# Kernel tuning notes

Measured on AMD Instinct MI355X. Metric: run time of the kernel, lower is better.

Reference implementation:

```python
import jax, jax.numpy as jnp
import numpy as np
import math

NUM_HEADS = 12


def _rope_tables(nph, npw, half_head_dim):
    # grid coords: x = column index, y = row index, flattened row-major
    rows = jnp.arange(nph, dtype=jnp.float32)
    cols = jnp.arange(npw, dtype=jnp.float32)
    gy, gx = jnp.meshgrid(rows, cols, indexing='ij')
    coords = jnp.stack([gx.ravel(), gy.ravel()], axis=1)  # [N, 2]
    cmin = coords.min(axis=0, keepdims=True)
    cmax = coords.max(axis=0, keepdims=True)
    nc = (coords - cmin) / (cmax - cmin + 1e-8)
    div = jnp.exp(jnp.arange(0, half_head_dim, 2, dtype=jnp.float32)
                  * (-(math.log(10000.0) / half_head_dim)))  # [half/2]
    px = nc[:, 0:1] * div  # [N, half/2]
    py = nc[:, 1:2] * div
    rep = lambda t: jnp.repeat(t, 2, axis=-1)  # interleave: even/odd slots get same value
    return rep(jnp.cos(px)), rep(jnp.sin(px)), rep(jnp.cos(py)), rep(jnp.sin(py))


def _apply_rope(t, cos_x, sin_x, cos_y, sin_y):
    # t: [B, H, N, Dh]; tables: [N, Dh//2] broadcast over B, H
    half = t.shape[-1] // 2
    tx, ty = t[..., :half], t[..., half:]
    rx = tx * cos_x + jnp.roll(tx, 1, axis=-1) * sin_x
    ry = ty * cos_y + jnp.roll(ty, 1, axis=-1) * sin_y
    return jnp.concatenate([rx, ry], axis=-1)


def setup_inputs() -> dict:
    key = jax.random.key(0)
    k1, k2, k3 = jax.random.split(key, 3)
    B, S, E = 32, 577, 768  # 24*24 patches + 1 CLS token
    x = jax.random.normal(k1, (B, S, E), dtype=jnp.float32)
    w_qkv = jax.random.normal(k2, (3 * E, E), dtype=jnp.float32) * 0.02
    w_proj = jax.random.normal(k3, (E, E), dtype=jnp.float32) * 0.02
    return {"x": x, "w_qkv": w_qkv, "w_proj": w_proj,
            "num_patches_h": 24, "num_patches_w": 24}


def reference(x, w_qkv, w_proj, num_patches_h, num_patches_w):
    B, S, E = x.shape
    H = NUM_HEADS
    Dh = E // H
    # QKV projection (bias=False)
    qkv = jnp.einsum('bse,fe->bsf', x, w_qkv).reshape(B, S, 3, H, Dh)
    qkv = jnp.transpose(qkv, (2, 0, 3, 1, 4))  # [3, B, H, S, Dh]
    q, k, v = qkv[0], qkv[1], qkv[2]
    # 2D RoPE on patch tokens only (CLS at position 0 unchanged)
    cx, sx, cy, sy = _rope_tables(num_patches_h, num_patches_w, Dh // 2)
    q_patch = _apply_rope(q[:, :, 1:], cx, sx, cy, sy)
    k_patch = _apply_rope(k[:, :, 1:], cx, sx, cy, sy)
    q = jnp.concatenate([q[:, :, :1], q_patch], axis=2)
    k = jnp.concatenate([k[:, :, :1], k_patch], axis=2)
    # scaled dot-product attention (standard backend, dropout=0)
    attn = jnp.einsum('bhqd,bhkd->bhqk', q, k) * (Dh ** -0.5)
    attn = jax.nn.softmax(attn, axis=-1)
    out = jnp.einsum('bhqk,bhkd->bhqd', attn, v)
    out = jnp.transpose(out, (0, 2, 1, 3)).reshape(B, S, E)
    return out @ w_proj.T
```

## Files before the change

### kernel.cpp

```cpp
#include <hip/hip_runtime.h>
#include <hip/hip_bf16.h>
#include <cstdint>


typedef __attribute__((ext_vector_type(8))) short bf16x8;
typedef __attribute__((ext_vector_type(4))) float f32x4;

#define MFMA16(a, b, c) __builtin_amdgcn_mfma_f32_16x16x32_bf16((a), (b), (c), 0, 0, 0)

#define S_LEN 577
#define NHEAD 12
#define DHEAD 64
#define EMB   768
#define F3    2304
#define NT_KV 10

__device__ __forceinline__ void gload_lds16(const __hip_bfloat16* g, __hip_bfloat16* l) {
    __builtin_amdgcn_global_load_lds(
        (const __attribute__((address_space(1))) unsigned int*)g,
        (__attribute__((address_space(3))) unsigned int*)l, 16, 0, 0);
}

__device__ __forceinline__ uint4 load8_f32(const float* p) {
    const float4 f0 = *(const float4*)p;
    const float4 f1 = *(const float4*)(p + 4);
    union { uint4 u; __hip_bfloat16 h[8]; } r;
    r.h[0] = __float2bfloat16(f0.x); r.h[1] = __float2bfloat16(f0.y);
    r.h[2] = __float2bfloat16(f0.z); r.h[3] = __float2bfloat16(f0.w);
    r.h[4] = __float2bfloat16(f1.x); r.h[5] = __float2bfloat16(f1.y);
    r.h[6] = __float2bfloat16(f1.z); r.h[7] = __float2bfloat16(f1.w);
    return r.u;
}

__global__ __launch_bounds__(256) void cvt_f32_bf16(
    const float* __restrict__ src, __hip_bfloat16* __restrict__ dst, int n8)
{
    const int i = blockIdx.x * 256 + threadIdx.x;
    if (i < n8)
        *(uint4*)(dst + (size_t)i * 8) = load8_f32(src + (size_t)i * 8);
}

template<bool BF32, bool CF32>
__global__ __launch_bounds__(256) void gemm_a_dma(
    const __hip_bfloat16* __restrict__ A, int lda,
    const void* __restrict__ Bv, int ldb,
    void* __restrict__ Cv, int M, int N, int K)
{
    __shared__ __hip_bfloat16 As[128 * 32];
    __shared__ __hip_bfloat16 Bs[128 * 32];

    const int t      = threadIdx.x;
    const int l      = t & 63;
    const int w      = t >> 6;
    const int lane15 = l & 15;
    const int quad   = l >> 4;

    const int n0 = blockIdx.x * 128;
    const int m0 = blockIdx.y * 128;
    const int wm = (w >> 1) * 64;
    const int wn = (w & 1) * 64;

    const int srow   = t >> 2;
    const int schunk = t & 3;
    const int fsw    = (t >> 3) & 3;
    const int gchunk = schunk ^ fsw;

    int ar0 = m0 + srow;       if (ar0 > M - 1) ar0 = M - 1;
    int ar1 = m0 + 64 + srow;  if (ar1 > M - 1) ar1 = M - 1;
    const int br0 = n0 + srow;
    const int br1 = n0 + 64 + srow;

    const __hip_bfloat16* pa0 = A + (size_t)ar0 * lda + gchunk * 8;
    const __hip_bfloat16* pa1 = A + (size_t)ar1 * lda + gchunk * 8;
    const size_t b0off = (size_t)br0 * ldb + gchunk * 8;
    const size_t b1off = (size_t)br1 * ldb + gchunk * 8;

    __hip_bfloat16* lAs0 = As + srow * 32 + schunk * 8;
    __hip_bfloat16* lAs1 = As + (64 + srow) * 32 + schunk * 8;
    __hip_bfloat16* lBs0 = Bs + srow * 32 + schunk * 8;
    __hip_bfloat16* lBs1 = Bs + (64 + srow) * 32 + schunk * 8;

    const int rsw = (quad ^ ((lane15 >> 1) & 3)) * 8;

    f32x4 acc[4][4] = {};

    for (int k0 = 0; k0 < K; k0 += 32) {
        uint4 vb0, vb1;
        if constexpr (BF32) {
            vb0 = load8_f32((const float*)Bv + b0off + k0);
            vb1 = load8_f32((const float*)Bv + b1off + k0);
        }
        __syncthreads();
        gload_lds16(pa0 + k0, lAs0);
        gload_lds16(pa1 + k0, lAs1);
        if constexpr (BF32) {
            *(uint4*)lBs0 = vb0;
            *(uint4*)lBs1 = vb1;
        } else {
            gload_lds16((const __hip_bfloat16*)Bv + b0off + k0, lBs0);
            gload_lds16((const __hip_bfloat16*)Bv + b1off + k0, lBs1);
        }
        __syncthreads();

        bf16x8 a[4], b[4];
        #pragma unroll
        for (int i = 0; i < 4; ++i)
            a[i] = *(const bf16x8*)(As + (wm + i * 16 + lane15) * 32 + rsw);
        #pragma unroll
        for (int j = 0; j < 4; ++j)
            b[j] = *(const bf16x8*)(Bs + (wn + j * 16 + lane15) * 32 + rsw);

        #pragma unroll
        for (int i = 0; i < 4; ++i)
            #pragma unroll
            for (int j = 0; j < 4; ++j)
                acc[i][j] = MFMA16(a[i], b[j], acc[i][j]);
    }

    #pragma unroll
    for (int i = 0; i < 4; ++i) {
        #pragma unroll
        for (int r = 0; r < 4; ++r) {
            const int m = m0 + wm + i * 16 + quad * 4 + r;
            if (m < M) {
                #pragma unroll
                for (int j = 0; j < 4; ++j) {
                    const int n = n0 + wn + j * 16 + lane15;
                    if constexpr (CF32)
                        ((float*)Cv)[(size_t)m * N + n] = acc[i][j][r];
                    else
                        ((__hip_bfloat16*)Cv)[(size_t)m * N + n] = __float2bfloat16(acc[i][j][r]);
                }
            }
        }
    }
}

__global__ __launch_bounds__(256) void rope_kernel(__hip_bfloat16* __restrict__ qkv)
{
    const int p = blockIdx.x;
    const int b = blockIdx.y;
    const int l = threadIdx.x & 63;
    const int w = threadIdx.x >> 6;

    const int jj   = l & 31;
    const float i2 = (float)((jj >> 1) * 2);
    const float dv = __expf(-i2 * 0.28782313662425576f);
    const float inv = 1.0f / (23.0f + 1e-8f);
    const float cx = (float)(p % 24) * inv;
    const float cy = (float)(p / 24) * inv;
    const float ang = ((l < 32) ? cx : cy) * dv;
    const float c = __cosf(ang);
    const float s = __sinf(ang);
    const int nb = (l & 32) | ((jj + 31) & 31);

    const size_t rowbase = ((size_t)(b * S_LEN + 1 + p)) * F3;

    for (int pr = w; pr < 24; pr += 4) {
        const int part = pr / 12;
        const int h    = pr % 12;
        const size_t off = rowbase + (size_t)part * EMB + h * DHEAD + l;
        float v  = __bfloat162float(qkv[off]);
        float vp = __shfl(v, nb, 64);
        qkv[off] = __float2bfloat16(v * c + vp * s);
    }
}

__global__ __launch_bounds__(512) void attn_kernel(
    const __hip_bfloat16* __restrict__ qkv,
    __hip_bfloat16* __restrict__ attn_out, int ldo)
{
    __shared__ __hip_bfloat16 Qs[128][72];
    __shared__ __hip_bfloat16 Ks[64][72];
    __shared__ __hip_bfloat16 Vt[64][72];

    const int t      = threadIdx.x;
    const int l      = t & 63;
    const int w      = t >> 6;
    const int lane15 = l & 15;
    const int quad   = l >> 4;

    const int q0 = blockIdx.x * 128;
    const int h  = blockIdx.y;
    const int b  = blockIdx.z;

    const int krow = t >> 3, kseg = t & 7;
    const int vs   = t & 63, vdg = t >> 6;

    uint4 ku, vu;
    {
        int gk = krow; if (gk > S_LEN - 1) gk = S_LEN - 1;
        ku = ((const uint4*)(qkv + (size_t)(b * S_LEN + gk) * F3 + EMB + h * DHEAD))[kseg];
        int gv = vs;  if (gv > S_LEN - 1) gv = S_LEN - 1;
        vu = ((const uint4*)(qkv + (size_t)(b * S_LEN + gv) * F3 + 2 * EMB + h * DHEAD))[vdg];
    }

    {
        const int row = t >> 2, seg = t & 3;
        int gq = q0 + row; if (gq > S_LEN - 1) gq = S_LEN - 1;
        const uint4* src = (const uint4*)(qkv + (size_t)(b * S_LEN + gq) * F3 + h * DHEAD + seg * 16);
        uint4 u0 = src[0], u1 = src[1];
        const __hip_bfloat16* e0 = (const __hip_bfloat16*)&u0;
        const __hip_bfloat16* e1 = (const __hip_bfloat16*)&u1;
        #pragma unroll
        for (int i = 0; i < 8; ++i) {
            Qs[row][seg * 16 + i]     = __float2bfloat16(__bfloat162float(e0[i]) * 0.125f);
            Qs[row][seg * 16 + 8 + i] = __float2bfloat16(__bfloat162float(e1[i]) * 0.125f);
        }
    }
    __syncthreads();

    bf16x8 qf0 = *(const bf16x8*)&Qs[w * 16 + lane15][quad * 8];
    bf16x8 qf1 = *(const bf16x8*)&Qs[w * 16 + lane15][32 + quad * 8];

    f32x4 o[4] = {};
    float m_i = -3.0e38f;
    float l_i = 0.f;

    for (int ti = 0; ti < NT_KV; ++ti) {
        __syncthreads();
        *(uint4*)&Ks[krow][kseg * 8] = ku;
        {
            const __hip_bfloat16* e0 = (const __hip_bfloat16*)&vu;
            #pragma unroll
            for (int i = 0; i < 8; ++i)
                Vt[vdg * 8 + i][vs] = e0[i];
        }
        if (ti + 1 < NT_KV) {
            int gk = (ti + 1) * 64 + krow; if (gk > S_LEN - 1) gk = S_LEN - 1;
            ku = ((const uint4*)(qkv + (size_t)(b * S_LEN + gk) * F3 + EMB + h * DHEAD))[kseg];
            int gv = (ti + 1) * 64 + vs;  if (gv > S_LEN - 1) gv = S_LEN - 1;
            vu = ((const uint4*)(qkv + (size_t)(b * S_LEN + gv) * F3 + 2 * EMB + h * DHEAD))[vdg];
        }
        asm volatile("s_waitcnt lgkmcnt(0)" ::: "memory");
        __builtin_amdgcn_s_barrier();
        asm volatile("" ::: "memory");

        f32x4 sf[4];
        #pragma unroll
        for (int nt = 0; nt < 4; ++nt) {
            f32x4 z = {0.f, 0.f, 0.f, 0.f};
            bf16x8 k0f = *(const bf16x8*)&Ks[nt * 16 + lane15][quad * 8];
            bf16x8 k1f = *(const bf16x8*)&Ks[nt * 16 + lane15][32 + quad * 8];
            z = MFMA16(k0f, qf0, z);
            z = MFMA16(k1f, qf1, z);
            sf[nt] = z;
        }
        const int s0 = ti * 64;
        #pragma unroll
        for (int nt = 0; nt < 4; ++nt)
            #pragma unroll
            for (int r = 0; r < 4; ++r)
                if (s0 + nt * 16 + quad * 4 + r >= S_LEN) sf[nt][r] = -1e30f;

        float mx = fmaxf(fmaxf(sf[0][0], sf[0][1]), fmaxf(sf[0][2], sf[0][3]));
        #pragma unroll
        for (int nt = 1; nt < 4; ++nt)
            mx = fmaxf(mx, fmaxf(fmaxf(sf[nt][0], sf[nt][1]), fmaxf(sf[nt][2], sf[nt][3])));
        mx = fmaxf(mx, __shfl_xor(mx, 16, 64));
        mx = fmaxf(mx, __shfl_xor(mx, 32, 64));

        const float mnew  = fmaxf(m_i, mx);
        const float alpha = __expf(m_i - mnew);
        m_i = mnew;

        float sum = 0.f;
        #pragma unroll
        for (int nt = 0; nt < 4; ++nt) {
            #pragma unroll
            for (int r = 0; r < 4; ++r) {
                sf[nt][r] = __expf(sf[nt][r] - mnew);
                sum += sf[nt][r];
            }
        }
        sum += __shfl_xor(sum, 16, 64);
        sum += __shfl_xor(sum, 32, 64);
        l_i = l_i * alpha + sum;

        float af[4];
        #pragma unroll
        for (int r = 0; r < 4; ++r)
            af[r] = __shfl(alpha, quad * 4 + r, 64);
        #pragma unroll
        for (int ci = 0; ci < 4; ++ci)
            #pragma unroll
            for (int r = 0; r < 4; ++r)
                o[ci][r] *= af[r];

        #pragma unroll
        for (int nt = 0; nt < 4; ++nt)
            #pragma unroll
            for (int r = 0; r < 4; ++r)
                Qs[w * 16 + lane15][nt * 16 + quad * 4 + r] = __float2bfloat16(sf[nt][r]);
        asm volatile("s_waitcnt lgkmcnt(0)" ::: "memory");

        #pragma unroll
        for (int s32 = 0; s32 < 2; ++s32) {
            bf16x8 pa = *(const bf16x8*)&Qs[w * 16 + lane15][s32 * 32 + quad * 8];
            #pragma unroll
            for (int ci = 0; ci < 4; ++ci) {
                bf16x8 vb = *(const bf16x8*)&Vt[ci * 16 + lane15][s32 * 32 + quad * 8];
                o[ci] = MFMA16(pa, vb, o[ci]);
            }
        }
    }

    #pragma unroll
    for (int r = 0; r < 4; ++r) {
        const float lr = __shfl(l_i, quad * 4 + r, 64);
        const int q = q0 + w * 16 + quad * 4 + r;
        if (q < S_LEN) {
            const float rl = 1.0f / lr;
            #pragma unroll
            for (int ci = 0; ci < 4; ++ci) {
                attn_out[(size_t)(b * S_LEN + q) * ldo + h * DHEAD + ci * 16 + lane15] =
                    __float2bfloat16(o[ci][r] * rl);
            }
        }
    }
}

extern "C" void kernel_launch(void* const* d_in, const int* in_sizes, int n_in,
                              void* d_out, int out_size, void* d_ws, size_t ws_size,
                              hipStream_t stream) {
    const float* x      = (const float*)d_in[0];
    const float* w_qkv  = (const float*)d_in[1];
    const float* w_proj = (const float*)d_in[2];
    for (int i = 0; i < n_in; ++i) {
        if      (in_sizes[i] == 32 * S_LEN * EMB) x      = (const float*)d_in[i];
        else if (in_sizes[i] == F3 * EMB)         w_qkv  = (const float*)d_in[i];
        else if (in_sizes[i] == EMB * EMB)        w_proj = (const float*)d_in[i];
    }
    float* out = (float*)d_out;

    const int Mrows = 32 * S_LEN;
    const int NX    = Mrows * EMB;
    const int NWQ   = F3 * EMB;

    __hip_bfloat16* qkv = (__hip_bfloat16*)d_ws;
    __hip_bfloat16* xb  = (__hip_bfloat16*)d_out;
    __hip_bfloat16* wb  = xb + (size_t)NX;

    cvt_f32_bf16<<<NX / 8 / 256, 256, 0, stream>>>(x, xb, NX / 8);
    cvt_f32_bf16<<<NWQ / 8 / 256, 256, 0, stream>>>(w_qkv, wb, NWQ / 8);
    gemm_a_dma<false, false><<<dim3(F3 / 128, (Mrows + 127) / 128), 256, 0, stream>>>(
        xb, EMB, wb, EMB, qkv, Mrows, F3, EMB);
    rope_kernel<<<dim3(576, 32), 256, 0, stream>>>(qkv);
    attn_kernel<<<dim3((S_LEN + 127) / 128, NHEAD, 32), 512, 0, stream>>>(qkv, qkv, F3);
    gemm_a_dma<true, true><<<dim3(EMB / 128, (Mrows + 127) / 128), 256, 0, stream>>>(
        qkv, F3, w_proj, EMB, out, Mrows, EMB, EMB);
}
```

Baseline: 378.8 us.

## Double-buffer LDS tiles in GEMM to overlap global loads with MFMA

Converts the GEMM main loop to a ping-pong LDS scheme: the next K-tile's A (via global-to-LDS DMA) and B loads are issued before the current tile's MFMAs, and fp32 B values are converted and stored after compute. This removes one of two barriers per iteration and hides global-load latency behind matrix math. It doubles LDS usage per block, which may reduce occupancy. It also assumes K is a multiple of 64.

```diff
diff --git a/kernel.cpp b/kernel.cpp
--- a/kernel.cpp
+++ b/kernel.cpp
@@ -14,6 +14,7 @@
 #define EMB   768
 #define F3    2304
 #define NT_KV 10
+#define BUFO  (128 * 32)
 
 __device__ __forceinline__ void gload_lds16(const __hip_bfloat16* g, __hip_bfloat16* l) {
     __builtin_amdgcn_global_load_lds(
@@ -21,15 +22,17 @@
         (__attribute__((address_space(3))) unsigned int*)l, 16, 0, 0);
 }
 
+__device__ __forceinline__ uint4 cvt8_f32(float4 a, float4 b) {
+    union { uint4 u; __hip_bfloat16 h[8]; } r;
+    r.h[0] = __float2bfloat16(a.x); r.h[1] = __float2bfloat16(a.y);
+    r.h[2] = __float2bfloat16(a.z); r.h[3] = __float2bfloat16(a.w);
+    r.h[4] = __float2bfloat16(b.x); r.h[5] = __float2bfloat16(b.y);
+    r.h[6] = __float2bfloat16(b.z); r.h[7] = __float2bfloat16(b.w);
+    return r.u;
+}
+
 __device__ __forceinline__ uint4 load8_f32(const float* p) {
-    const float4 f0 = *(const float4*)p;
-    const float4 f1 = *(const float4*)(p + 4);
-    union { uint4 u; __hip_bfloat16 h[8]; } r;
-    r.h[0] = __float2bfloat16(f0.x); r.h[1] = __float2bfloat16(f0.y);
-    r.h[2] = __float2bfloat16(f0.z); r.h[3] = __float2bfloat16(f0.w);
-    r.h[4] = __float2bfloat16(f1.x); r.h[5] = __float2bfloat16(f1.y);
-    r.h[6] = __float2bfloat16(f1.z); r.h[7] = __float2bfloat16(f1.w);
-    return r.u;
+    return cvt8_f32(*(const float4*)p, *(const float4*)(p + 4));
 }
 
 __global__ __launch_bounds__(256) void cvt_f32_bf16(
@@ -46,8 +49,8 @@
     const void* __restrict__ Bv, int ldb,
     void* __restrict__ Cv, int M, int N, int K)
 {
-    __shared__ __hip_bfloat16 As[128 * 32];
-    __shared__ __hip_bfloat16 Bs[128 * 32];
+    __shared__ __hip_bfloat16 As[2 * BUFO];
+    __shared__ __hip_bfloat16 Bs[2 * BUFO];
 
     const int t      = threadIdx.x;
     const int l      = t & 63;
@@ -84,38 +87,60 @@
 
     f32x4 acc[4][4] = {};
 
-    for (int k0 = 0; k0 < K; k0 += 32) {
-        uint4 vb0, vb1;
-        if constexpr (BF32) {
-            vb0 = load8_f32((const float*)Bv + b0off + k0);
-            vb1 = load8_f32((const float*)Bv + b1off + k0);
-        }
-        __syncthreads();
-        gload_lds16(pa0 + k0, lAs0);
-        gload_lds16(pa1 + k0, lAs1);
-        if constexpr (BF32) {
-            *(uint4*)lBs0 = vb0;
-            *(uint4*)lBs1 = vb1;
-        } else {
-            gload_lds16((const __hip_bfloat16*)Bv + b0off + k0, lBs0);
-            gload_lds16((const __hip_bfloat16*)Bv + b1off + k0, lBs1);
-        }
-        __syncthreads();
-
-        bf16x8 a[4], b[4];
-        #pragma unroll
-        for (int i = 0; i < 4; ++i)
-            a[i] = *(const bf16x8*)(As + (wm + i * 16 + lane15) * 32 + rsw);
-        #pragma unroll
-        for (int j = 0; j < 4; ++j)
-            b[j] = *(const bf16x8*)(Bs + (wn + j * 16 + lane15) * 32 + rsw);
-
-        #pragma unroll
-        for (int i = 0; i < 4; ++i)
-            #pragma unroll
-            for (int j = 0; j < 4; ++j)
-                acc[i][j] = MFMA16(a[i], b[j], acc[i][j]);
-    }
+    gload_lds16(pa0, lAs0);
+    gload_lds16(pa1, lAs1);
+    if constexpr (BF32) {
+        *(uint4*)lBs0 = load8_f32((const float*)Bv + b0off);
+        *(uint4*)lBs1 = load8_f32((const float*)Bv + b1off);
+    } else {
+        gload_lds16((const __hip_bfloat16*)Bv + b0off, lBs0);
+        gload_lds16((const __hip_bfloat16*)Bv + b1off, lBs1);
+    }
+    __syncthreads();
+
+#define GEMM_STEP(kn, CO, NO)                                                 \
+    {                                                                         \
+        float4 g0 = {}, g1 = {}, g2 = {}, g3 = {};                            \
+        const bool has_next = (kn) < K;                                       \
+        if (has_next) {                                                       \
+            gload_lds16(pa0 + (kn), lAs0 + (NO));                             \
+            gload_lds16(pa1 + (kn), lAs1 + (NO));                             \
+            if constexpr (BF32) {                                             \
+                const float* pb0 = (const float*)Bv + b0off + (kn);           \
+                const float* pb1 = (const float*)Bv + b1off + (kn);           \
+                g0 = *(const float4*)pb0; g1 = *(const float4*)(pb0 + 4);     \
+                g2 = *(const float4*)pb1; g3 = *(const float4*)(pb1 + 4);     \
+            } else {                                                          \
+                gload_lds16((const __hip_bfloat16*)Bv + b0off + (kn), lBs0 + (NO)); \
+                gload_lds16((const __hip_bfloat16*)Bv + b1off + (kn), lBs1 + (NO)); \
+            }                                                                 \
+        }                                                                     \
+        bf16x8 a[4], b[4];                                                    \
+        _Pragma("unroll")                                                     \
+        for (int i = 0; i < 4; ++i)                                           \
+            a[i] = *(const bf16x8*)(As + (CO) + (wm + i * 16 + lane15) * 32 + rsw); \
+        _Pragma("unroll")                                                     \
+        for (int j = 0; j < 4; ++j)                                           \
+            b[j] = *(const bf16x8*)(Bs + (CO) + (wn + j * 16 + lane15) * 32 + rsw); \
+        _Pragma("unroll")                                                     \
+        for (int i = 0; i < 4; ++i)                                           \
+            _Pragma("unroll")                                                 \
+            for (int j = 0; j < 4; ++j)                                       \
+                acc[i][j] = MFMA16(a[i], b[j], acc[i][j]);                    \
+        if constexpr (BF32) {                                                 \
+            if (has_next) {                                                   \
+                *(uint4*)(lBs0 + (NO)) = cvt8_f32(g0, g1);                    \
+                *(uint4*)(lBs1 + (NO)) = cvt8_f32(g2, g3);                    \
+            }                                                                 \
+        }                                                                     \
+        __syncthreads();                                                      \
+    }
+
+    for (int k0 = 0; k0 < K; k0 += 64) {
+        GEMM_STEP(k0 + 32, 0,    BUFO)
+        GEMM_STEP(k0 + 64, BUFO, 0)
+    }
+#undef GEMM_STEP
 
     #pragma unroll
     for (int i = 0; i < 4; ++i) {
```

Result: slower. 395.8 us (+4.5%).
